# Kernel optimization log

Hardware: AMD Instinct MI355X
Metric: run time of the kernel (lower is better)

## Reference

```python
import jax, jax.numpy as jnp
import numpy as np

EPS = 1e-5
PATCH_SIZES = [None, 13]
PATCH_WEIGHTS = [0.5, 0.5]


def _box(x, p):
    # sliding-window sum over spatial dims, VALID padding -> [B,C,H-p+1,W-p+1]
    return jax.lax.reduce_window(x, 0.0, jax.lax.add, (1, 1, p, p), (1, 1, 1, 1), 'VALID')


def _global_ncc(x1, x2):
    # InstanceNorm2d (biased var, eps) per (b,c) over spatial dims, then dot / (c*h*w)
    b, c, h, w = x1.shape
    m1 = jnp.mean(x1, axis=(2, 3), keepdims=True)
    m2 = jnp.mean(x2, axis=(2, 3), keepdims=True)
    v1 = jnp.mean((x1 - m1) ** 2, axis=(2, 3), keepdims=True)
    v2 = jnp.mean((x2 - m2) ** 2, axis=(2, 3), keepdims=True)
    n1 = (x1 - m1) * jax.lax.rsqrt(v1 + EPS)
    n2 = (x2 - m2) * jax.lax.rsqrt(v2 + EPS)
    return jnp.sum(n1 * n2, axis=(1, 2, 3)) / (c * h * w)


def _patch_ncc(x1, x2, p):
    # Equivalent fused form of: unfold -> rearrange (patch locations become
    # channels, pxp patch pixels become spatial) -> InstanceNorm2d -> dot.
    # Each pxp patch is normalized over its own pixels => local NCC.
    b, c, h, w = x1.shape
    n = p * p
    s1 = _box(x1, p)
    s2 = _box(x2, p)
    s11 = _box(x1 * x1, p)
    s22 = _box(x2 * x2, p)
    s12 = _box(x1 * x2, p)
    m1 = s1 / n
    m2 = s2 / n
    v1 = s11 / n - m1 * m1  # biased variance, matches InstanceNorm2d
    v2 = s22 / n - m2 * m2
    cross = s12 - n * m1 * m2  # sum_p (I-mI)(J-mJ)
    cc = cross * jax.lax.rsqrt((v1 + EPS) * (v2 + EPS))  # [B,C,H',W']
    hp, wp = h - p + 1, w - p + 1
    # original divides by (channels' * h' * w') where channels' = c*hp*wp, spatial = p*p
    return jnp.sum(cc, axis=(1, 2, 3)) / (c * hp * wp * n)


def setup_inputs() -> dict:
    key = jax.random.key(0)
    k1, k2 = jax.random.split(key)
    x1 = jax.random.normal(k1, (32, 1, 512, 512), dtype=jnp.float32)
    x2 = jax.random.normal(k2, (32, 1, 512, 512), dtype=jnp.float32)
    return {"x1": x1, "x2": x2}


def reference(x1, x2):
    scores = []
    for w, p in zip(PATCH_WEIGHTS, PATCH_SIZES):
        if p is None:
            scores.append(w * _global_ncc(x1, x2))
        else:
            scores.append(w * _patch_ncc(x1, x2, p))
    return jnp.stack(scores, axis=0).sum(axis=0)  # [B]
```

## Files before the change

### kernel.cpp

```cpp
#include <hip/hip_runtime.h>

#define EPS 1e-5f

typedef float v2f __attribute__((ext_vector_type(2)));

constexpr int B = 32;
constexpr int H = 512;
constexpr int W = 512;
constexpr int NPIX = H * W;
constexpr int P = 13;
constexpr int HP = H - P + 1;
constexpr int WP = W - P + 1;
constexpr int TILES_X = 4;
constexpr int BAND_OUT = 40;
constexpr int BANDS_Y = 13;
constexpr int G = 13;
constexpr int NGROUPS = 4;
constexpr int ITER_LAST_OWN = 20;
constexpr int ITER_LAST_EMIT = 32;
constexpr int BLOCKS_PER_B = TILES_X * BANDS_Y;
constexpr int RS = 140;

#define GLOAD_LDS16(gp, lp)                                                    \
  __builtin_amdgcn_global_load_lds(                                            \
      (const __attribute__((address_space(1))) unsigned int*)(const void*)(gp),\
      (__attribute__((address_space(3))) unsigned int*)(void*)(lp), 16, 0, 0)

__global__ __launch_bounds__(64) void ncc_fused_kernel(
    const float* __restrict__ x1, const float* __restrict__ x2,
    float* __restrict__ part) {
  const int bid = blockIdx.x;
  const int b    = bid / BLOCKS_PER_B;
  const int rem  = bid % BLOCKS_PER_B;
  const int tile = rem % TILES_X;
  const int band = rem / TILES_X;
  const bool last = (band == BANDS_Y - 1);
  const int x0 = tile * 128;
  const int y0 = last ? (HP - BAND_OUT) : band * BAND_OUT;
  const int tid = threadIdx.x;
  const int c0 = x0 + 2 * tid;
  const bool valid0 = c0 < WP;
  const bool valid1 = (c0 + 1) < WP;

  __shared__ float sa[2][G][RS];
  __shared__ float sb[2][G][RS];

  const float* r1 = x1 + (size_t)b * NPIX + (size_t)y0 * W + x0;
  const float* r2 = x2 + (size_t)b * NPIX + (size_t)y0 * W + x0;

  int qoff = tid * 4;
  { int mx = W - x0 - 4; if (qoff > mx) qoff = mx; }
  const bool loader = tid < 35;

  auto stage = [&](int g, int buf) {
    if (loader) {
#pragma unroll
      for (int r = 0; r < G; ++r) {
        GLOAD_LDS16(r1 + (size_t)(g * G + r) * W + qoff, &sa[buf][r][0]);
        GLOAD_LDS16(r2 + (size_t)(g * G + r) * W + qoff, &sb[buf][r][0]);
      }
    }
  };

  v2f rr1[G], rr2[G], rr11[G], rr22[G], rr12[G];
  v2f S1 = {0.f, 0.f}, S2 = {0.f, 0.f}, S11 = {0.f, 0.f}, S22 = {0.f, 0.f},
      S12 = {0.f, 0.f};
  v2f g1 = {0.f, 0.f}, g2 = {0.f, 0.f}, g11 = {0.f, 0.f}, g22 = {0.f, 0.f},
      g12 = {0.f, 0.f};
  float acc = 0.f;
  const float inv_n = 1.0f / 169.0f;

  auto step = [&](int u, int buf, int t, bool fill) {
    const float* pa = &sa[buf][u][2 * tid];
    const float* pb = &sb[buf][u][2 * tid];
    v2f A[7], Bv[7];
#pragma unroll
    for (int k = 0; k < 7; ++k) {
      A[k] = *(const v2f*)(pa + 2 * k);
      Bv[k] = *(const v2f*)(pb + 2 * k);
    }

    v2f q11 = A[0] * A[0], q22 = Bv[0] * Bv[0], q12 = A[0] * Bv[0];
    v2f h1v = A[0], h2v = Bv[0], h11v = q11, h22v = q22, h12v = q12;
#pragma unroll
    for (int k = 1; k < 6; ++k) {
      h1v += A[k];
      h2v += Bv[k];
      h11v += A[k] * A[k];
      h22v += Bv[k] * Bv[k];
      h12v += A[k] * Bv[k];
    }
    float a12 = A[6].x, b12 = Bv[6].x, a13 = A[6].y, b13 = Bv[6].y;
    float h1_0 = h1v.x + h1v.y + a12;
    float h2_0 = h2v.x + h2v.y + b12;
    float h11_0 = fmaf(a12, a12, h11v.x + h11v.y);
    float h22_0 = fmaf(b12, b12, h22v.x + h22v.y);
    float h12_0 = fmaf(a12, b12, h12v.x + h12v.y);
    v2f h1 = {h1_0, h1_0 - A[0].x + a13};
    v2f h2 = {h2_0, h2_0 - Bv[0].x + b13};
    v2f h11 = {h11_0, fmaf(a13, a13, h11_0 - q11.x)};
    v2f h22 = {h22_0, fmaf(b13, b13, h22_0 - q22.x)};
    v2f h12 = {h12_0, fmaf(a13, b13, h12_0 - q12.x)};

    bool owned = last ? (t >= ITER_LAST_OWN) : (t < BAND_OUT);
    if (owned) {
      g1 += A[0]; g2 += Bv[0]; g11 += q11; g22 += q22; g12 += q12;
    }

    if (fill) {
      S1 += h1; S2 += h2; S11 += h11; S22 += h22; S12 += h12;
    } else {
      S1 += h1 - rr1[u]; S2 += h2 - rr2[u];
      S11 += h11 - rr11[u]; S22 += h22 - rr22[u]; S12 += h12 - rr12[u];
    }
    rr1[u] = h1; rr2[u] = h2; rr11[u] = h11; rr22[u] = h22; rr12[u] = h12;

    bool do_out = (t >= 12) && (!last || t >= ITER_LAST_EMIT);
    if (do_out) {
      v2f m1 = S1 * inv_n, m2 = S2 * inv_n;
      v2f vv1 = S11 * inv_n - m1 * m1 + EPS;
      v2f vv2 = S22 * inv_n - m2 * m2 + EPS;
      v2f cross = S12 - (S1 * inv_n) * S2;
      v2f den = vv1 * vv2;
      float cc0 = cross.x * rsqrtf(den.x);
      float cc1 = cross.y * rsqrtf(den.y);
      acc += (valid0 ? cc0 : 0.f) + (valid1 ? cc1 : 0.f);
    }
  };

  stage(0, 0);
  __syncthreads();
  stage(1, 1);

#pragma unroll
  for (int u = 0; u < G; ++u) step(u, 0, u, true);
  __syncthreads();

#pragma clang loop unroll(disable)
  for (int g = 1; g < NGROUPS; ++g) {
    if (g + 1 < NGROUPS) stage(g + 1, (g + 1) & 1);
    const int buf = g & 1;
#pragma unroll
    for (int u = 0; u < G; ++u) step(u, buf, g * G + u, false);
    __syncthreads();
  }

  float v0 = acc;
  float w1 = g1.x + g1.y, w2 = g2.x + g2.y;
  float w3 = g11.x + g11.y, w4 = g22.x + g22.y, w5 = g12.x + g12.y;
#pragma unroll
  for (int off = 32; off > 0; off >>= 1) {
    v0 += __shfl_down(v0, off, 64);
    w1 += __shfl_down(w1, off, 64);
    w2 += __shfl_down(w2, off, 64);
    w3 += __shfl_down(w3, off, 64);
    w4 += __shfl_down(w4, off, 64);
    w5 += __shfl_down(w5, off, 64);
  }
  if (tid == 0) {
    float* o = part + (size_t)bid * 6;
    o[0] = v0; o[1] = w1; o[2] = w2; o[3] = w3; o[4] = w4; o[5] = w5;
  }
}

__global__ __launch_bounds__(64) void final_kernel(
    const float* __restrict__ part, float* __restrict__ out) {
  int b = blockIdx.x;
  int tid = threadIdx.x;
  float s[6] = {0.f, 0.f, 0.f, 0.f, 0.f, 0.f};
  for (int i = tid; i < BLOCKS_PER_B; i += 64) {
    const float* p = part + (size_t)(b * BLOCKS_PER_B + i) * 6;
#pragma unroll
    for (int k = 0; k < 6; ++k) s[k] += p[k];
  }
#pragma unroll
  for (int off = 32; off > 0; off >>= 1) {
#pragma unroll
    for (int k = 0; k < 6; ++k) s[k] += __shfl_down(s[k], off, 64);
  }
  if (tid == 0) {
    float Nf = (float)NPIX;
    float m1 = s[1] / Nf;
    float m2 = s[2] / Nf;
    float v1 = fmaf(-m1, m1, s[3] / Nf);
    float v2 = fmaf(-m2, m2, s[4] / Nf);
    float cross = fmaf(-Nf * m1, m2, s[5]);
    float g = cross * rsqrtf((v1 + EPS) * (v2 + EPS)) / Nf;
    float patch = s[0] / ((float)HP * (float)WP * 169.0f);
    out[b] = 0.5f * g + 0.5f * patch;
  }
}

extern "C" void kernel_launch(void* const* d_in, const int* in_sizes, int n_in,
                              void* d_out, int out_size, void* d_ws, size_t ws_size,
                              hipStream_t stream) {
  const float* x1 = (const float*)d_in[0];
  const float* x2 = (const float*)d_in[1];
  float* out = (float*)d_out;
  float* part = (float*)d_ws;

  ncc_fused_kernel<<<B * BLOCKS_PER_B, 64, 0, stream>>>(x1, x2, part);
  final_kernel<<<B, 64, 0, stream>>>(part, out);
}
```

Baseline: 121.4 us.

## Replace group double-buffering with per-row ring-buffer DMA and two waves per workgroup

Replaces the two-buffer, 13-row group staging and its block-wide barriers with a 13-slot ring buffer per wave. Each step issues the async global-to-LDS load for the row 13 ahead into the slot it just consumed, and a vmcnt wait gates each step instead of __syncthreads. Two independent waves now share a workgroup, each with its own LDS region, which halves the block count. This removes barrier stalls and keeps more loads in flight continuously. It relies on hand-written waitcnt counts being correct for ordering, and loads past the last row are clamped to redundant reloads.

```diff
diff --git a/kernel.cpp b/kernel.cpp
--- a/kernel.cpp
+++ b/kernel.cpp
@@ -11,14 +11,19 @@
 constexpr int P = 13;
 constexpr int HP = H - P + 1;
 constexpr int WP = W - P + 1;
+constexpr int TILE_W = 128;
 constexpr int TILES_X = 4;
+constexpr int WAVES = 2;
 constexpr int BAND_OUT = 40;
 constexpr int BANDS_Y = 13;
 constexpr int G = 13;
+constexpr int NROWS = 52;
 constexpr int NGROUPS = 4;
 constexpr int ITER_LAST_OWN = 20;
 constexpr int ITER_LAST_EMIT = 32;
-constexpr int BLOCKS_PER_B = TILES_X * BANDS_Y;
+constexpr int PAIRS_X = TILES_X / WAVES;
+constexpr int WGS_PER_B = PAIRS_X * BANDS_Y;
+constexpr int UNITS_PER_B = TILES_X * BANDS_Y;
 constexpr int RS = 140;
 
 #define GLOAD_LDS16(gp, lp)                                                    \
@@ -26,43 +31,53 @@
       (const __attribute__((address_space(1))) unsigned int*)(const void*)(gp),\
       (__attribute__((address_space(3))) unsigned int*)(void*)(lp), 16, 0, 0)
 
-__global__ __launch_bounds__(64) void ncc_fused_kernel(
+#define WAITV24() asm volatile("s_waitcnt vmcnt(24)" ::: "memory")
+
+__global__ __launch_bounds__(128) void ncc_fused_kernel(
     const float* __restrict__ x1, const float* __restrict__ x2,
     float* __restrict__ part) {
   const int bid = blockIdx.x;
-  const int b    = bid / BLOCKS_PER_B;
-  const int rem  = bid % BLOCKS_PER_B;
-  const int tile = rem % TILES_X;
-  const int band = rem / TILES_X;
+  const int b    = bid / WGS_PER_B;
+  const int rem  = bid % WGS_PER_B;
+  const int pair = rem % PAIRS_X;
+  const int band = rem / PAIRS_X;
   const bool last = (band == BANDS_Y - 1);
-  const int x0 = tile * 128;
+  const int w    = threadIdx.x >> 6;
+  const int lane = threadIdx.x & 63;
+  const int tile = pair * WAVES + w;
+  const int x0 = tile * TILE_W;
   const int y0 = last ? (HP - BAND_OUT) : band * BAND_OUT;
-  const int tid = threadIdx.x;
-  const int c0 = x0 + 2 * tid;
+  const int c0 = x0 + 2 * lane;
   const bool valid0 = c0 < WP;
   const bool valid1 = (c0 + 1) < WP;
 
-  __shared__ float sa[2][G][RS];
-  __shared__ float sb[2][G][RS];
+  __shared__ float sa[WAVES][G][RS];
+  __shared__ float sb[WAVES][G][RS];
 
   const float* r1 = x1 + (size_t)b * NPIX + (size_t)y0 * W + x0;
   const float* r2 = x2 + (size_t)b * NPIX + (size_t)y0 * W + x0;
 
-  int qoff = tid * 4;
+  int qoff = lane * 4;
   { int mx = W - x0 - 4; if (qoff > mx) qoff = mx; }
-  const bool loader = tid < 35;
-
-  auto stage = [&](int g, int buf) {
+  const bool loader = lane < 35;
+
+  auto dma_row = [&](int row, int slot) {
     if (loader) {
-#pragma unroll
-      for (int r = 0; r < G; ++r) {
-        GLOAD_LDS16(r1 + (size_t)(g * G + r) * W + qoff, &sa[buf][r][0]);
-        GLOAD_LDS16(r2 + (size_t)(g * G + r) * W + qoff, &sb[buf][r][0]);
-      }
+      GLOAD_LDS16(r1 + (size_t)row * W + qoff, &sa[w][slot][0]);
+      GLOAD_LDS16(r2 + (size_t)row * W + qoff, &sb[w][slot][0]);
     }
   };
 
+#pragma unroll
+  for (int r = 0; r < G; ++r) dma_row(r, r);
+
   v2f rr1[G], rr2[G], rr11[G], rr22[G], rr12[G];
+#pragma unroll
+  for (int u = 0; u < G; ++u) {
+    rr1[u] = (v2f){0.f, 0.f}; rr2[u] = (v2f){0.f, 0.f};
+    rr11[u] = (v2f){0.f, 0.f}; rr22[u] = (v2f){0.f, 0.f};
+    rr12[u] = (v2f){0.f, 0.f};
+  }
   v2f S1 = {0.f, 0.f}, S2 = {0.f, 0.f}, S11 = {0.f, 0.f}, S22 = {0.f, 0.f},
       S12 = {0.f, 0.f};
   v2f g1 = {0.f, 0.f}, g2 = {0.f, 0.f}, g11 = {0.f, 0.f}, g22 = {0.f, 0.f},
@@ -70,14 +85,20 @@
   float acc = 0.f;
   const float inv_n = 1.0f / 169.0f;
 
-  auto step = [&](int u, int buf, int t, bool fill) {
-    const float* pa = &sa[buf][u][2 * tid];
-    const float* pb = &sb[buf][u][2 * tid];
+  auto step = [&](int u, int t) {
+    const float* pa = &sa[w][u][2 * lane];
+    const float* pb = &sb[w][u][2 * lane];
     v2f A[7], Bv[7];
 #pragma unroll
     for (int k = 0; k < 7; ++k) {
       A[k] = *(const v2f*)(pa + 2 * k);
       Bv[k] = *(const v2f*)(pb + 2 * k);
+    }
+    asm volatile("s_waitcnt lgkmcnt(0)" ::: "memory");
+    {
+      int nrow = t + G;
+      if (nrow > NROWS - 1) nrow = NROWS - 1;
+      dma_row(nrow, u);
     }
 
     v2f q11 = A[0] * A[0], q22 = Bv[0] * Bv[0], q12 = A[0] * Bv[0];
@@ -107,12 +128,8 @@
       g1 += A[0]; g2 += Bv[0]; g11 += q11; g22 += q22; g12 += q12;
     }
 
-    if (fill) {
-      S1 += h1; S2 += h2; S11 += h11; S22 += h22; S12 += h12;
-    } else {
-      S1 += h1 - rr1[u]; S2 += h2 - rr2[u];
-      S11 += h11 - rr11[u]; S22 += h22 - rr22[u]; S12 += h12 - rr12[u];
-    }
+    S1 += h1 - rr1[u]; S2 += h2 - rr2[u];
+    S11 += h11 - rr11[u]; S22 += h22 - rr22[u]; S12 += h12 - rr12[u];
     rr1[u] = h1; rr2[u] = h2; rr11[u] = h11; rr22[u] = h22; rr12[u] = h12;
 
     bool do_out = (t >= 12) && (!last || t >= ITER_LAST_EMIT);
@@ -128,22 +145,16 @@
     }
   };
 
-  stage(0, 0);
-  __syncthreads();
-  stage(1, 1);
-
-#pragma unroll
-  for (int u = 0; u < G; ++u) step(u, 0, u, true);
-  __syncthreads();
-
 #pragma clang loop unroll(disable)
-  for (int g = 1; g < NGROUPS; ++g) {
-    if (g + 1 < NGROUPS) stage(g + 1, (g + 1) & 1);
-    const int buf = g & 1;
-#pragma unroll
-    for (int u = 0; u < G; ++u) step(u, buf, g * G + u, false);
-    __syncthreads();
-  }
+  for (int g = 0; g < NGROUPS; ++g) {
+#pragma unroll
+    for (int u = 0; u < G; ++u) {
+      WAITV24();
+      step(u, g * G + u);
+    }
+  }
+
+  asm volatile("s_waitcnt vmcnt(0)" ::: "memory");
 
   float v0 = acc;
   float w1 = g1.x + g1.y, w2 = g2.x + g2.y;
@@ -157,8 +168,8 @@
     w4 += __shfl_down(w4, off, 64);
     w5 += __shfl_down(w5, off, 64);
   }
-  if (tid == 0) {
-    float* o = part + (size_t)bid * 6;
+  if (lane == 0) {
+    float* o = part + (size_t)(bid * WAVES + w) * 6;
     o[0] = v0; o[1] = w1; o[2] = w2; o[3] = w3; o[4] = w4; o[5] = w5;
   }
 }
@@ -168,8 +179,8 @@
   int b = blockIdx.x;
   int tid = threadIdx.x;
   float s[6] = {0.f, 0.f, 0.f, 0.f, 0.f, 0.f};
-  for (int i = tid; i < BLOCKS_PER_B; i += 64) {
-    const float* p = part + (size_t)(b * BLOCKS_PER_B + i) * 6;
+  for (int i = tid; i < UNITS_PER_B; i += 64) {
+    const float* p = part + (size_t)(b * UNITS_PER_B + i) * 6;
 #pragma unroll
     for (int k = 0; k < 6; ++k) s[k] += p[k];
   }
@@ -199,6 +210,6 @@
   float* out = (float*)d_out;
   float* part = (float*)d_ws;
 
-  ncc_fused_kernel<<<B * BLOCKS_PER_B, 64, 0, stream>>>(x1, x2, part);
+  ncc_fused_kernel<<<B * WGS_PER_B, WAVES * 64, 0, stream>>>(x1, x2, part);
   final_kernel<<<B, 64, 0, stream>>>(part, out);
 }
```

New measurement: 113.1 us. 1.07x faster.
